# Performance work log

Hardware: AMD Instinct MI355X
Metric: run time of the kernel (lower is better)

The kernel has to match this reference:

```python
import jax, jax.numpy as jnp
import numpy as np

N, E, W_IN, W_OUT, NUM_CLASS, M = 4096, 5, 512, 128, 16, 1024
NUM_LAYERS, ALPHA, THETA = 64, 0.1, 0.5

def leaky_relu(x):
    return jnp.where(x >= 0, x, 0.01 * x)

def setup_inputs() -> dict:
    key = jax.random.key(0)
    ks = jax.random.split(key, 16)
    u = jax.random.uniform(ks[0], (N, N, E), jnp.float32)
    A = jnp.where(u < 0.01, u, 0.0)
    X = jax.random.normal(ks[1], (N, W_IN), jnp.float32)
    target_x = jax.random.randint(ks[2], (M,), 0, N)
    target = jax.random.randint(ks[3], (M,), 0, NUM_CLASS)
    def xav(k, shape):
        fan_in, fan_out = shape[-2], shape[-1]
        lim = (6.0 / (fan_in + fan_out)) ** 0.5
        return jax.random.uniform(k, shape, jnp.float32, -lim, lim)
    H0 = W_IN + E * W_OUT  # DGCN input width
    return dict(
        A=A, X=X, target_x=target_x, target=target,
        weight=xav(ks[4], (W_IN, W_OUT)),
        attw=xav(ks[5], (1, N)),
        attb=jnp.zeros((1, W_OUT), jnp.float32),
        attq=xav(ks[6], (1, W_OUT)),
        Wg=xav(ks[7], (W_IN, W_IN)), bg=jnp.zeros((W_IN,), jnp.float32),
        W0=xav(ks[8], (H0, W_OUT)), b0=jnp.zeros((W_OUT,), jnp.float32),
        Wconvs=xav(ks[9], (NUM_LAYERS, W_OUT, W_OUT)),
        Wd1=xav(ks[10], (W_OUT, W_OUT)), bd1=jnp.zeros((W_OUT,), jnp.float32),
        W1=xav(ks[11], (W_OUT, W_OUT)), b1=jnp.zeros((W_OUT,), jnp.float32),
        W2=xav(ks[12], (W_OUT, NUM_CLASS)), b2=jnp.zeros((NUM_CLASS,), jnp.float32),
    )

def reference(A, X, target_x, target, weight, attw, attb, attq, Wg, bg, W0, b0,
              Wconvs, Wd1, bd1, W1, b1, W2, b2):
    Ae = jnp.transpose(A, (2, 0, 1))              # [E,N,N]
    I = jnp.eye(N, dtype=A.dtype)
    # gcn_conv feature transform is identical for every edge type (dropout p=0)
    Xw = leaky_relu(leaky_relu(X @ Wg + bg) @ weight)   # [N, w_out]
    # norm(H, add=True): transpose, set diagonal to 1, row-normalize by degree
    Ht = Ae.transpose(0, 2, 1) * (1.0 - I) + I          # [E,N,N]
    deg = Ht.sum(-1)
    dinv = jnp.where(deg > 0, 1.0 / deg, 0.0)
    lgcn = jax.nn.relu(jnp.einsum('enm,md->end', dinv[..., None] * Ht, Xw))  # [E,N,w_out]
    # edge-type attention
    tm = jnp.tanh(jnp.einsum('n,end->ed', attw[0], lgcn) + attb)  # [E,w_out]
    watt = (tm * attq[0]).sum(-1)                                  # [E]
    beta = jax.nn.softmax(watt) * E
    Xcat = (beta[:, None, None] * lgcn).transpose(1, 0, 2).reshape(N, E * W_OUT)
    X_ = jnp.concatenate([Xcat, X], axis=1)       # [N, w_in + E*w_out]
    # DGCN: GCNII stack on binary nonzero pattern of mean adjacency, gcn_norm
    B = (jnp.mean(Ae, 0) != 0).astype(A.dtype)
    Bs = jnp.maximum(B, I)                        # add remaining self-loops
    d = Bs.sum(1)
    dis = jnp.where(d > 0, jax.lax.rsqrt(d), 0.0)
    A_hat = dis[:, None] * Bs * dis[None, :]      # D^-1/2 (B+I) D^-1/2
    x0 = jax.nn.relu(X_ @ W0 + b0)                # [N, w_out]
    betas_l = jnp.log(THETA / jnp.arange(1, NUM_LAYERS + 1, dtype=A.dtype) + 1.0)
    def step(x, inp):
        Wl, bl = inp
        h = A_hat @ x
        h = (1.0 - ALPHA) * h + ALPHA * x0        # initial residual
        x = jax.nn.relu((1.0 - bl) * h + bl * (h @ Wl))  # identity mapping
        return x, None
    x, _ = jax.lax.scan(step, x0, (Wconvs, betas_l))
    Z = leaky_relu(x @ Wd1 + bd1)                 # DGCN lins[1] + outer leaky_relu
    Z = leaky_relu(Z @ W1 + b1)                   # linear1
    y = Z[target_x] @ W2 + b2                     # linear2 on labeled nodes [M,C]
    logp = jax.nn.log_softmax(y, axis=-1)
    loss = -jnp.mean(jnp.take_along_axis(logp, target[:, None], axis=1))
    return loss, y
```

## Files before the change

kernel.cpp:

```cpp
#include <hip/hip_runtime.h>
#include <cstdint>
#include <cmath>

#define NN   4096
#define EE   5
#define WIN  512
#define WOUT 128
#define HH0  1152
#define NLAY 64
#define NCLS 16
#define MT   1024
#define GCAP 96
#define BCAP 320
#define ECAP 48
#define KSPLIT 8
#define KCHUNK 512
#define NTILE  8

typedef __attribute__((ext_vector_type(8))) short     bf16x8_t;
typedef __attribute__((ext_vector_type(8))) unsigned short ushort8_t;
typedef __attribute__((ext_vector_type(4))) float     f32x4_t;

__device__ inline unsigned short f2bf(float f) {
  unsigned int u = __float_as_uint(f);
  unsigned int r = (u + 0x7FFFu + ((u >> 16) & 1u)) >> 16;
  return (unsigned short)r;
}

__device__ __forceinline__ void gload16(const unsigned short* g, unsigned short* l) {
  __builtin_amdgcn_global_load_lds(
      (__attribute__((address_space(1))) void*)g,
      (__attribute__((address_space(3))) void*)l, 16, 0, 0);
}

__global__ __launch_bounds__(256) void gemm_kernel(
    const float* __restrict__ A, const float* __restrict__ W,
    const float* __restrict__ bias, float* __restrict__ C,
    int Mdim, int Kdim, int Ndim, int act) {
  __shared__ __align__(16) float sA[16][68];
  __shared__ __align__(16) float sW[16][64];
  int tid = threadIdx.x;
  int tx = tid & 15, ty = tid >> 4;
  int row0 = blockIdx.y * 64, col0 = blockIdx.x * 64;
  float acc[4][4] = {};
  int mA = tid >> 2;
  int kA = (tid & 3) << 2;
  int kW = tid >> 4;
  int nW = (tid & 15) << 2;
  for (int k0 = 0; k0 < Kdim; k0 += 16) {
    float4 av = *(const float4*)(A + (size_t)(row0 + mA) * Kdim + k0 + kA);
    float4 wv = *(const float4*)(W + (size_t)(k0 + kW) * Ndim + col0 + nW);
    sA[kA + 0][mA] = av.x;
    sA[kA + 1][mA] = av.y;
    sA[kA + 2][mA] = av.z;
    sA[kA + 3][mA] = av.w;
    *(float4*)&sW[kW][nW] = wv;
    __syncthreads();
#pragma unroll
    for (int kk = 0; kk < 16; kk++) {
      float4 a = *(const float4*)&sA[kk][ty << 2];
      float4 b = *(const float4*)&sW[kk][tx << 2];
      acc[0][0] += a.x * b.x; acc[0][1] += a.x * b.y; acc[0][2] += a.x * b.z; acc[0][3] += a.x * b.w;
      acc[1][0] += a.y * b.x; acc[1][1] += a.y * b.y; acc[1][2] += a.y * b.z; acc[1][3] += a.y * b.w;
      acc[2][0] += a.z * b.x; acc[2][1] += a.z * b.y; acc[2][2] += a.z * b.z; acc[2][3] += a.z * b.w;
      acc[3][0] += a.w * b.x; acc[3][1] += a.w * b.y; acc[3][2] += a.w * b.z; acc[3][3] += a.w * b.w;
    }
    __syncthreads();
  }
#pragma unroll
  for (int i = 0; i < 4; i++) {
    int r = row0 + (ty << 2) + i;
#pragma unroll
    for (int jc = 0; jc < 4; jc++) {
      int c = col0 + (tx << 2) + jc;
      float o = acc[i][jc];
      if (bias) o += bias[c];
      if (act == 1) o = fmaxf(o, 0.f);
      else if (act == 2) o = (o >= 0.f) ? o : 0.01f * o;
      C[(size_t)r * Ndim + c] = o;
    }
  }
}

__global__ __launch_bounds__(256) void scan_rows_kernel(
    const float* __restrict__ A, int* __restrict__ fcnt, int* __restrict__ fidx,
    float* __restrict__ fval, int* __restrict__ bcnt, int* __restrict__ bidx) {
  __shared__ int   lbuf[1024];
  __shared__ int   lcnt;
  __shared__ int   ecnt[EE];
  __shared__ int   en2[EE][ECAP];
  __shared__ float ev[EE][ECAP];
  __shared__ int   rbase;
  __shared__ int   gbase[EE];
  int tid = threadIdx.x;
  int n1 = blockIdx.x >> 2;
  int qb = (blockIdx.x & 3) << 10;
  if (tid == 0) lcnt = 0;
  if (tid < EE) ecnt[tid] = 0;
  __syncthreads();
  const float4* src = (const float4*)(A + ((size_t)n1 * NN + qb) * EE);
  float buf[20];
  float4* bf4 = (float4*)buf;
#pragma unroll
  for (int c = 0; c < 5; c++) bf4[c] = src[tid * 5 + c];
  int n2base = qb + tid * 4;
#pragma unroll
  for (int u = 0; u < 4; u++) {
    int n2 = n2base + u;
    if (n2 == n1) continue;
    bool any = false;
#pragma unroll
    for (int e = 0; e < EE; e++) {
      float v = buf[u * 5 + e];
      if (v != 0.f) {
        any = true;
        int s = atomicAdd(&ecnt[e], 1);
        if (s < ECAP) { en2[e][s] = n2; ev[e][s] = v; }
      }
    }
    if (any) {
      int s = atomicAdd(&lcnt, 1);
      lbuf[s] = n2;
    }
  }
  __syncthreads();
  if (tid == 0) rbase = atomicAdd(&bcnt[n1], lcnt);
  if (tid < EE) gbase[tid] = atomicAdd(&fcnt[tid * NN + n1], min(ecnt[tid], ECAP));
  __syncthreads();
  int c = lcnt, rb = rbase;
  for (int s = tid; s < c; s += 256)
    if (rb + s < BCAP) bidx[(size_t)n1 * BCAP + rb + s] = lbuf[s];
#pragma unroll
  for (int e = 0; e < EE; e++) {
    int ec = min(ecnt[e], ECAP), gb = gbase[e];
    size_t base = ((size_t)e * NN + n1) * GCAP;
    for (int s = tid; s < ec; s += 256) {
      if (gb + s < GCAP) {
        fidx[base + gb + s] = en2[e][s];
        fval[base + gb + s] = ev[e][s];
      }
    }
  }
}

__global__ __launch_bounds__(64) void transpose_kernel(
    const int* __restrict__ fcnt, const int* __restrict__ fidx, const float* __restrict__ fval,
    int* __restrict__ gcnt, int* __restrict__ gidx, float* __restrict__ gval) {
  int id = blockIdx.x;
  int n1 = id & (NN - 1);
  int e  = id >> 12;
  int c = min(fcnt[id], GCAP);
  for (int s = threadIdx.x; s < c; s += 64) {
    int   n2 = fidx[(size_t)id * GCAP + s];
    float v  = fval[(size_t)id * GCAP + s];
    int t = e * NN + n2;
    int slot = atomicAdd(&gcnt[t], 1);
    if (slot < GCAP) {
      gidx[(size_t)t * GCAP + slot] = n1;
      gval[(size_t)t * GCAP + slot] = v;
    }
  }
}

__global__ void dinv_dis_kernel(const int* __restrict__ gcnt, const float* __restrict__ gval,
                                float* __restrict__ dinv, const int* __restrict__ bcnt,
                                float* __restrict__ dis) {
  int t = blockIdx.x * 256 + threadIdx.x;
  if (t < EE * NN) {
    int cnt = min(gcnt[t], GCAP);
    float s = 1.0f;
    for (int k = 0; k < cnt; k++) s += gval[(size_t)t * GCAP + k];
    dinv[t] = 1.0f / s;
  }
  if (t < NN) dis[t] = rsqrtf(1.0f + (float)min(bcnt[t], BCAP));
}

__global__ __launch_bounds__(256) void build_ahat_kernel(
    const int* __restrict__ bcnt, const int* __restrict__ bidx,
    const float* __restrict__ dis, unsigned short* __restrict__ Ab) {
  __shared__ unsigned int bits[128];
  int i = blockIdx.x, t = threadIdx.x;
  if (t < 128) bits[t] = 0;
  __syncthreads();
  int cnt = min(bcnt[i], BCAP);
  for (int s = t; s < cnt; s += 256) {
    int j = bidx[(size_t)i * BCAP + s];
    atomicOr(&bits[j >> 5], 1u << (j & 31));
  }
  __syncthreads();
  float di = dis[i];
  int c0 = t * 16;
  unsigned short out[16];
#pragma unroll
  for (int u = 0; u < 16; u++) {
    int j = c0 + u;
    bool on = ((bits[j >> 5] >> (j & 31)) & 1u) || (j == i);
    out[u] = on ? f2bf(di * dis[j]) : (unsigned short)0;
  }
  *(ushort8_t*)&Ab[(size_t)i * NN + c0]     = *(ushort8_t*)&out[0];
  *(ushort8_t*)&Ab[(size_t)i * NN + c0 + 8] = *(ushort8_t*)&out[8];
}

__global__ __launch_bounds__(128) void lgcn_kernel(
    const int* __restrict__ gcnt, const int* __restrict__ gidx, const float* __restrict__ gval,
    const float* __restrict__ dinv, const float* __restrict__ Xw, float* __restrict__ lgcn) {
  int i = blockIdx.x, e = blockIdx.y, d = threadIdx.x;
  int t = e * NN + i;
  int cnt = min(gcnt[t], GCAP);
  __shared__ int   sj[GCAP];
  __shared__ float sv[GCAP];
  for (int s = d; s < cnt; s += 128) {
    sj[s] = gidx[(size_t)t * GCAP + s];
    sv[s] = gval[(size_t)t * GCAP + s];
  }
  __syncthreads();
  float acc = Xw[(size_t)i * WOUT + d];
  for (int s = 0; s < cnt; s++) acc += sv[s] * Xw[(size_t)sj[s] * WOUT + d];
  float r = dinv[t] * acc;
  lgcn[(size_t)t * WOUT + d] = fmaxf(r, 0.f);
}

__global__ void att_partial_kernel(const float* __restrict__ lgcn, const float* __restrict__ attw,
                                   float* __restrict__ tm_pre) {
  int e = blockIdx.y, d = threadIdx.x;
  int nbase = blockIdx.x * 128;
  float acc = 0.f;
  for (int k = 0; k < 128; k++) {
    int n = nbase + k;
    acc += attw[n] * lgcn[((size_t)(e * NN + n)) * WOUT + d];
  }
  atomicAdd(&tm_pre[e * WOUT + d], acc);
}

__global__ void att_final_kernel(const float* __restrict__ tm_pre, const float* __restrict__ attb,
                                 const float* __restrict__ attq, float* __restrict__ beta) {
  int lane = threadIdx.x;
  __shared__ float sw[EE];
  for (int e = 0; e < EE; e++) {
    float v = 0.f;
    for (int d = lane; d < WOUT; d += 64) {
      float tmv = tanhf(tm_pre[e * WOUT + d] + attb[d]);
      v += tmv * attq[d];
    }
    for (int off = 32; off; off >>= 1) v += __shfl_down(v, off, 64);
    if (lane == 0) sw[e] = v;
  }
  __syncthreads();
  if (lane == 0) {
    float mx = sw[0];
    for (int e = 1; e < EE; e++) mx = fmaxf(mx, sw[e]);
    float se = 0.f, ex[EE];
    for (int e = 0; e < EE; e++) { ex[e] = expf(sw[e] - mx); se += ex[e]; }
    for (int e = 0; e < EE; e++) beta[e] = ex[e] / se * (float)EE;
  }
}

__global__ void xcat_kernel(const float* __restrict__ lgcn, const float* __restrict__ X,
                            const float* __restrict__ beta, float* __restrict__ Xc) {
  int idx = blockIdx.x * 256 + threadIdx.x;
  const int total = NN * HH0;
  for (; idx < total; idx += gridDim.x * 256) {
    int n = idx / HH0, c = idx - n * HH0;
    float v;
    if (c < EE * WOUT) {
      int e = c >> 7, d = c & 127;
      v = beta[e] * lgcn[((size_t)(e * NN + n)) * WOUT + d];
    } else {
      v = X[(size_t)n * WIN + (c - EE * WOUT)];
    }
    Xc[idx] = v;
  }
}

__global__ __launch_bounds__(256) void xT_convert_kernel(
    const float* __restrict__ x, unsigned short* __restrict__ xT) {
  __shared__ float sh2[128][36];
  int r0 = blockIdx.x * 32, t = threadIdx.x;
  const float4* x4 = (const float4*)(x + (size_t)r0 * WOUT);
#pragma unroll
  for (int q = 0; q < 4; q++) {
    int lin = t + q * 256;
    int r = lin >> 5, c = (lin & 31) * 4;
    float4 v = x4[lin];
    sh2[c + 0][r] = v.x; sh2[c + 1][r] = v.y; sh2[c + 2][r] = v.z; sh2[c + 3][r] = v.w;
  }
  __syncthreads();
  int c = t >> 1, half = t & 1;
  unsigned short tmp[16];
#pragma unroll
  for (int rr = 0; rr < 16; rr++) tmp[rr] = f2bf(sh2[c][half * 16 + rr]);
  *(ushort8_t*)&xT[(size_t)c * NN + r0 + half * 16]     = *(ushort8_t*)&tmp[0];
  *(ushort8_t*)&xT[(size_t)c * NN + r0 + half * 16 + 8] = *(ushort8_t*)&tmp[8];
}

__global__ __launch_bounds__(256) void spmm_kernel(
    const unsigned short* __restrict__ Ab, const unsigned short* __restrict__ xbT,
    float* __restrict__ P) {
  __shared__ __align__(16) unsigned short sT[2][12288];
  int t = threadIdx.x;
  int rt = blockIdx.x & 63, kc = blockIdx.x >> 6;
  int r0 = rt * 64, k0 = kc * KCHUNK;
  int wave = t >> 6, lane = t & 63;
  int wr = (wave & 1) * 32, wc = (wave >> 1) * 64;
  int quad = lane >> 4, mrow = lane & 15;
  f32x4_t acc[2][4] = {};

  const unsigned short* gq[6];
  int lq[6];
#pragma unroll
  for (int q = 0; q < 6; q++) {
    int c = wave * 6 + q;
    if (c < 8) {
      int sub = c >> 2, rb = c & 3;
      gq[q] = Ab + (size_t)(r0 + rb * 16 + (lane >> 2)) * NN + k0 + sub * 32 + (lane & 3) * 8;
      lq[q] = sub * 2048 + rb * 512;
    } else {
      int cc = c - 8;
      int sub = cc >> 3, rb = cc & 7;
      gq[q] = xbT + (size_t)(rb * 16 + (lane >> 2)) * NN + k0 + sub * 32 + (lane & 3) * 8;
      lq[q] = 4096 + sub * 4096 + rb * 512;
    }
  }

#define STAGE(BUF, TS)                                         \
  {                                                            \
    unsigned short* lb = &sT[(BUF)][0];                        \
    _Pragma("unroll")                                          \
    for (int q = 0; q < 6; q++)                                \
      gload16(gq[q] + (TS) * 64, lb + lq[q]);                  \
  }

  STAGE(0, 0);
  asm volatile("s_waitcnt vmcnt(0)" ::: "memory");
  __builtin_amdgcn_s_barrier();

  int cur = 0;
  for (int tt = 0; tt < NTILE; tt++) {
    if (tt < NTILE - 1) STAGE(cur ^ 1, tt + 1);
    const unsigned short* base = &sT[cur][0];
    bf16x8_t af[2][2], bfv[2][4];
#pragma unroll
    for (int kk = 0; kk < 2; kk++) {
#pragma unroll
      for (int mi = 0; mi < 2; mi++)
        af[kk][mi] = *(const bf16x8_t*)&base[kk * 2048 + (wr + mi * 16 + mrow) * 32 + quad * 8];
#pragma unroll
      for (int nj = 0; nj < 4; nj++)
        bfv[kk][nj] = *(const bf16x8_t*)&base[4096 + kk * 4096 + (wc + nj * 16 + mrow) * 32 + quad * 8];
    }
#pragma unroll
    for (int kk = 0; kk < 2; kk++)
#pragma unroll
      for (int mi = 0; mi < 2; mi++)
#pragma unroll
        for (int nj = 0; nj < 4; nj++)
          acc[mi][nj] = __builtin_amdgcn_mfma_f32_16x16x32_bf16(af[kk][mi], bfv[kk][nj], acc[mi][nj], 0, 0, 0);
    if (tt < NTILE - 1) {
      asm volatile("s_waitcnt vmcnt(0)" ::: "memory");
      __builtin_amdgcn_s_barrier();
      cur ^= 1;
    }
  }
#undef STAGE

  float* Pk = P + (size_t)kc * (NN * WOUT);
#pragma unroll
  for (int mi = 0; mi < 2; mi++)
#pragma unroll
    for (int nj = 0; nj < 4; nj++) {
#pragma unroll
      for (int r4 = 0; r4 < 4; r4++) {
        int row = r0 + wr + mi * 16 + quad * 4 + r4;
        int col = wc + nj * 16 + mrow;
        Pk[(size_t)row * WOUT + col] = acc[mi][nj][r4];
      }
    }
}

__global__ __launch_bounds__(256) void gcnii_epi_kernel(
    const float* __restrict__ P, const float* __restrict__ x0,
    const float* __restrict__ Wl, float bl,
    float* __restrict__ xout_f32, unsigned short* __restrict__ xoutT, int write_f32) {
  __shared__ float sh2[128][22];
  int r0 = blockIdx.x * 16, t = threadIdx.x;
#pragma unroll
  for (int q = 0; q < 2; q++) {
    int lin = t + q * 256;
    int r = lin >> 5, c = (lin & 31) * 4;
    size_t base4 = ((size_t)(r0 + r) * WOUT + c) >> 2;
    float4 s = {0.f, 0.f, 0.f, 0.f};
#pragma unroll
    for (int kc = 0; kc < KSPLIT; kc++) {
      float4 p = ((const float4*)P)[(size_t)kc * (NN * WOUT / 4) + base4];
      s.x += p.x; s.y += p.y; s.z += p.z; s.w += p.w;
    }
    float4 xv = ((const float4*)x0)[base4];
    s.x = 0.9f * s.x + 0.1f * xv.x;
    s.y = 0.9f * s.y + 0.1f * xv.y;
    s.z = 0.9f * s.z + 0.1f * xv.z;
    s.w = 0.9f * s.w + 0.1f * xv.w;
    sh2[c + 0][r] = s.x; sh2[c + 1][r] = s.y; sh2[c + 2][r] = s.z; sh2[c + 3][r] = s.w;
  }
  __syncthreads();
  int tx = t & 31, ty = t >> 5;
  float2 hv[4];
#pragma unroll
  for (int j = 0; j < 4; j++) hv[j] = *(const float2*)&sh2[tx * 4 + j][ty * 2];
  float o[2][4] = {};
  for (int k = 0; k < WOUT; k++) {
    float2 a = *(const float2*)&sh2[k][ty * 2];
    float4 w = *(const float4*)&Wl[k * WOUT + tx * 4];
    o[0][0] += a.x * w.x; o[0][1] += a.x * w.y; o[0][2] += a.x * w.z; o[0][3] += a.x * w.w;
    o[1][0] += a.y * w.x; o[1][1] += a.y * w.y; o[1][2] += a.y * w.z; o[1][3] += a.y * w.w;
  }
  float c1 = 1.f - bl;
  float y[2][4];
  float hvv[2][4] = {{hv[0].x, hv[1].x, hv[2].x, hv[3].x},
                     {hv[0].y, hv[1].y, hv[2].y, hv[3].y}};
#pragma unroll
  for (int i = 0; i < 2; i++)
#pragma unroll
    for (int j = 0; j < 4; j++)
      y[i][j] = fmaxf(c1 * hvv[i][j] + bl * o[i][j], 0.f);
  if (write_f32) {
#pragma unroll
    for (int i = 0; i < 2; i++) {
      float4 v = {y[i][0], y[i][1], y[i][2], y[i][3]};
      *(float4*)&xout_f32[(size_t)(r0 + ty * 2 + i) * WOUT + tx * 4] = v;
    }
  }
  __syncthreads();
#pragma unroll
  for (int i = 0; i < 2; i++)
#pragma unroll
    for (int j = 0; j < 4; j++)
      sh2[tx * 4 + j][ty * 2 + i] = y[i][j];
  __syncthreads();
  int c = t >> 1, half = t & 1;
  unsigned short tmp[8];
#pragma unroll
  for (int rr = 0; rr < 8; rr++) tmp[rr] = f2bf(sh2[c][half * 8 + rr]);
  *(ushort8_t*)&xoutT[(size_t)c * NN + r0 + half * 8] = *(ushort8_t*)&tmp[0];
}

__global__ __launch_bounds__(256) void head_kernel(
    const float* __restrict__ Z, const int* __restrict__ txv, const int* __restrict__ tgt,
    const float* __restrict__ W2, const float* __restrict__ b2,
    float* __restrict__ out_y, float* __restrict__ lossp) {
  int tid = threadIdx.x;
  int mr = tid >> 4, c = tid & 15;
  int m = blockIdx.x * 16 + mr;
  const float* zr = Z + (size_t)txv[m] * WOUT;
  float acc = b2[c];
  for (int k = 0; k < WOUT; k++) acc += zr[k] * W2[k * NCLS + c];
  out_y[(size_t)m * NCLS + c] = acc;
  float mx = acc;
  for (int off = 8; off; off >>= 1) mx = fmaxf(mx, __shfl_xor(mx, off, 16));
  float ex = expf(acc - mx);
  float se = ex;
  for (int off = 8; off; off >>= 1) se += __shfl_xor(se, off, 16);
  float lse = mx + logf(se);
  float contrib = (c == tgt[m]) ? (lse - acc) : 0.f;
  __shared__ float red[256];
  red[tid] = contrib;
  __syncthreads();
  for (int stp = 128; stp; stp >>= 1) {
    if (tid < stp) red[tid] += red[tid + stp];
    __syncthreads();
  }
  if (tid == 0) lossp[blockIdx.x] = red[0];
}

__global__ void loss_final_kernel(const float* __restrict__ lossp, float* __restrict__ out_loss) {
  int lane = threadIdx.x;
  float v = (lane < 64) ? lossp[lane] : 0.f;
  for (int off = 32; off; off >>= 1) v += __shfl_down(v, off, 64);
  if (lane == 0) out_loss[0] = v / (float)MT;
}

extern "C" void kernel_launch(void* const* d_in, const int* in_sizes, int n_in,
                              void* d_out, int out_size, void* d_ws, size_t ws_size,
                              hipStream_t stream) {
  const float* A      = (const float*)d_in[0];
  const float* X      = (const float*)d_in[1];
  const int*   txv    = (const int*)d_in[2];
  const int*   tgt    = (const int*)d_in[3];
  const float* weight = (const float*)d_in[4];
  const float* attw   = (const float*)d_in[5];
  const float* attb   = (const float*)d_in[6];
  const float* attq   = (const float*)d_in[7];
  const float* Wg     = (const float*)d_in[8];
  const float* bg     = (const float*)d_in[9];
  const float* W0     = (const float*)d_in[10];
  const float* b0     = (const float*)d_in[11];
  const float* Wconvs = (const float*)d_in[12];
  const float* Wd1    = (const float*)d_in[13];
  const float* bd1    = (const float*)d_in[14];
  const float* W1     = (const float*)d_in[15];
  const float* b1     = (const float*)d_in[16];
  const float* W2     = (const float*)d_in[17];
  const float* b2     = (const float*)d_in[18];

  float* ws  = (float*)d_ws;
  int*   wsi = (int*)d_ws;

  const size_t O_GCNT  = 0;
  const size_t O_BCNT  = 20480;
  const size_t O_FCNT  = 24576;
  const size_t O_DINV  = 45056;
  const size_t O_DIS   = 65536;
  const size_t O_TMPRE = 69632;
  const size_t O_BETA  = 70272;
  const size_t O_LOSSP = 70288;
  const size_t O_GIDX  = 71680;
  const size_t O_GVAL  = O_GIDX + 1966080;
  const size_t O_FIDX  = O_GVAL + 1966080;
  const size_t O_FVAL  = O_FIDX + 1966080;
  const size_t O_BIDX  = O_FVAL + 1966080;
  const size_t O_LGCN  = O_BIDX + 1310720;
  const size_t O_XW    = O_LGCN + 2621440;
  const size_t O_X0    = O_XW   + 524288;
  const size_t O_XA    = O_X0   + 524288;
  const size_t O_XB    = O_XA   + 524288;
  const size_t O_AB    = O_XB   + 524288;
  const size_t O_XBT0  = O_AB   + 8388608;
  const size_t O_XBT1  = O_XBT0 + 262144;
  const size_t O_P     = O_XBT1 + 262144;
  const size_t O_T1    = O_FVAL;
  const size_t O_XCAT  = O_GIDX;

  hipMemsetAsync(ws + O_GCNT, 0, 45056 * 4, stream);
  hipMemsetAsync(ws + O_TMPRE, 0, 640 * 4, stream);

  dim3 blk(256);
  gemm_kernel<<<dim3(WIN / 64, NN / 64), blk, 0, stream>>>(X, Wg, bg, ws + O_T1, NN, WIN, WIN, 2);
  gemm_kernel<<<dim3(WOUT / 64, NN / 64), blk, 0, stream>>>(ws + O_T1, weight, nullptr, ws + O_XW, NN, WIN, WOUT, 2);
  scan_rows_kernel<<<NN * 4, 256, 0, stream>>>(A, wsi + O_FCNT, wsi + O_FIDX, ws + O_FVAL,
                                               wsi + O_BCNT, wsi + O_BIDX);
  transpose_kernel<<<EE * NN, 64, 0, stream>>>(wsi + O_FCNT, wsi + O_FIDX, ws + O_FVAL,
                                               wsi + O_GCNT, wsi + O_GIDX, ws + O_GVAL);
  dinv_dis_kernel<<<80, 256, 0, stream>>>(wsi + O_GCNT, ws + O_GVAL, ws + O_DINV,
                                          wsi + O_BCNT, ws + O_DIS);
  build_ahat_kernel<<<NN, 256, 0, stream>>>(wsi + O_BCNT, wsi + O_BIDX, ws + O_DIS,
                                            (unsigned short*)(ws + O_AB));
  lgcn_kernel<<<dim3(NN, EE), 128, 0, stream>>>(wsi + O_GCNT, wsi + O_GIDX, ws + O_GVAL,
                                                ws + O_DINV, ws + O_XW, ws + O_LGCN);
  att_partial_kernel<<<dim3(32, EE), 128, 0, stream>>>(ws + O_LGCN, attw, ws + O_TMPRE);
  att_final_kernel<<<1, 64, 0, stream>>>(ws + O_TMPRE, attb, attq, ws + O_BETA);
  xcat_kernel<<<4096, 256, 0, stream>>>(ws + O_LGCN, X, ws + O_BETA, ws + O_XCAT);
  gemm_kernel<<<dim3(WOUT / 64, NN / 64), blk, 0, stream>>>(ws + O_XCAT, W0, b0, ws + O_X0, NN, HH0, WOUT, 1);
  xT_convert_kernel<<<NN / 32, 256, 0, stream>>>(ws + O_X0, (unsigned short*)(ws + O_XBT0));
  for (int l = 0; l < NLAY; l++) {
    float bl = logf(0.5f / (float)(l + 1) + 1.0f);
    const unsigned short* xin = (const unsigned short*)(ws + ((l & 1) ? O_XBT1 : O_XBT0));
    unsigned short* xoT = (unsigned short*)(ws + ((l & 1) ? O_XBT0 : O_XBT1));
    spmm_kernel<<<64 * KSPLIT, 256, 0, stream>>>((const unsigned short*)(ws + O_AB), xin, ws + O_P);
    gcnii_epi_kernel<<<NN / 16, 256, 0, stream>>>(ws + O_P, ws + O_X0,
                                                  Wconvs + (size_t)l * WOUT * WOUT, bl,
                                                  ws + O_XA, xoT, (l == NLAY - 1) ? 1 : 0);
  }
  gemm_kernel<<<dim3(WOUT / 64, NN / 64), blk, 0, stream>>>(ws + O_XA, Wd1, bd1, ws + O_XB, NN, WOUT, WOUT, 2);
  gemm_kernel<<<dim3(WOUT / 64, NN / 64), blk, 0, stream>>>(ws + O_XB, W1, b1, ws + O_X0, NN, WOUT, WOUT, 2);
  head_kernel<<<MT / 16, 256, 0, stream>>>(ws + O_X0, txv, tgt, W2, b2,
                                           (float*)d_out + 1, ws + O_LOSSP);
  loss_final_kernel<<<1, 64, 0, stream>>>(ws + O_LOSSP, (float*)d_out);
}
```

Before: 2.386 ms.

## Replace dense bf16 A_hat with bitmap and fold D^-1/2 scaling into features

Instead of materializing the dense normalized adjacency in bf16 (32 MB) and streaming it every layer, the normalization D^-1/2 (B+I) D^-1/2 is factored. The binary pattern is stored as a 2 MB bitmap that the SpMM kernel expands into bf16 ones and zeros in shared memory, and the column scaling dis[j] is applied to x when writing the transposed bf16 input. The row scaling dis[i] is applied in the epilogue. This cuts the per-layer HBM traffic for A by about 16x, at the cost of extra ALU work for bitmap expansion and a full __syncthreads in place of the explicit waitcnt barrier.

```diff
diff --git a/kernel.cpp b/kernel.cpp
--- a/kernel.cpp
+++ b/kernel.cpp
@@ -175,9 +175,9 @@
   if (t < NN) dis[t] = rsqrtf(1.0f + (float)min(bcnt[t], BCAP));
 }
 
-__global__ __launch_bounds__(256) void build_ahat_kernel(
+__global__ __launch_bounds__(256) void build_bitmap_kernel(
     const int* __restrict__ bcnt, const int* __restrict__ bidx,
-    const float* __restrict__ dis, unsigned short* __restrict__ Ab) {
+    unsigned int* __restrict__ bm) {
   __shared__ unsigned int bits[128];
   int i = blockIdx.x, t = threadIdx.x;
   if (t < 128) bits[t] = 0;
@@ -187,18 +187,9 @@
     int j = bidx[(size_t)i * BCAP + s];
     atomicOr(&bits[j >> 5], 1u << (j & 31));
   }
-  __syncthreads();
-  float di = dis[i];
-  int c0 = t * 16;
-  unsigned short out[16];
-#pragma unroll
-  for (int u = 0; u < 16; u++) {
-    int j = c0 + u;
-    bool on = ((bits[j >> 5] >> (j & 31)) & 1u) || (j == i);
-    out[u] = on ? f2bf(di * dis[j]) : (unsigned short)0;
-  }
-  *(ushort8_t*)&Ab[(size_t)i * NN + c0]     = *(ushort8_t*)&out[0];
-  *(ushort8_t*)&Ab[(size_t)i * NN + c0 + 8] = *(ushort8_t*)&out[8];
+  if (t == 0) atomicOr(&bits[i >> 5], 1u << (i & 31));
+  __syncthreads();
+  if (t < 128) bm[(size_t)i * 128 + t] = bits[t];
 }
 
 __global__ __launch_bounds__(128) void lgcn_kernel(
@@ -273,9 +264,12 @@
 }
 
 __global__ __launch_bounds__(256) void xT_convert_kernel(
-    const float* __restrict__ x, unsigned short* __restrict__ xT) {
+    const float* __restrict__ x, const float* __restrict__ dis,
+    unsigned short* __restrict__ xT) {
   __shared__ float sh2[128][36];
+  __shared__ float sdis[32];
   int r0 = blockIdx.x * 32, t = threadIdx.x;
+  if (t < 32) sdis[t] = dis[r0 + t];
   const float4* x4 = (const float4*)(x + (size_t)r0 * WOUT);
 #pragma unroll
   for (int q = 0; q < 4; q++) {
@@ -288,65 +282,85 @@
   int c = t >> 1, half = t & 1;
   unsigned short tmp[16];
 #pragma unroll
-  for (int rr = 0; rr < 16; rr++) tmp[rr] = f2bf(sh2[c][half * 16 + rr]);
+  for (int rr = 0; rr < 16; rr++)
+    tmp[rr] = f2bf(sdis[half * 16 + rr] * sh2[c][half * 16 + rr]);
   *(ushort8_t*)&xT[(size_t)c * NN + r0 + half * 16]     = *(ushort8_t*)&tmp[0];
   *(ushort8_t*)&xT[(size_t)c * NN + r0 + half * 16 + 8] = *(ushort8_t*)&tmp[8];
 }
 
 __global__ __launch_bounds__(256) void spmm_kernel(
-    const unsigned short* __restrict__ Ab, const unsigned short* __restrict__ xbT,
+    const unsigned int* __restrict__ bm, const unsigned short* __restrict__ xbT,
     float* __restrict__ P) {
-  __shared__ __align__(16) unsigned short sT[2][12288];
+  __shared__ __align__(16) unsigned short sX[2][2][128 * 32];
+  __shared__ __align__(16) unsigned short sA[2][2][64 * 32];
+  __shared__ __align__(16) unsigned int   sBM[64][16];
   int t = threadIdx.x;
   int rt = blockIdx.x & 63, kc = blockIdx.x >> 6;
   int r0 = rt * 64, k0 = kc * KCHUNK;
   int wave = t >> 6, lane = t & 63;
   int wr = (wave & 1) * 32, wc = (wave >> 1) * 64;
   int quad = lane >> 4, mrow = lane & 15;
+  int er = t >> 2, eq = t & 3;
   f32x4_t acc[2][4] = {};
 
-  const unsigned short* gq[6];
-  int lq[6];
-#pragma unroll
-  for (int q = 0; q < 6; q++) {
-    int c = wave * 6 + q;
-    if (c < 8) {
-      int sub = c >> 2, rb = c & 3;
-      gq[q] = Ab + (size_t)(r0 + rb * 16 + (lane >> 2)) * NN + k0 + sub * 32 + (lane & 3) * 8;
-      lq[q] = sub * 2048 + rb * 512;
-    } else {
-      int cc = c - 8;
-      int sub = cc >> 3, rb = cc & 7;
-      gq[q] = xbT + (size_t)(rb * 16 + (lane >> 2)) * NN + k0 + sub * 32 + (lane & 3) * 8;
-      lq[q] = 4096 + sub * 4096 + rb * 512;
-    }
-  }
-
-#define STAGE(BUF, TS)                                         \
-  {                                                            \
-    unsigned short* lb = &sT[(BUF)][0];                        \
-    _Pragma("unroll")                                          \
-    for (int q = 0; q < 6; q++)                                \
-      gload16(gq[q] + (TS) * 64, lb + lq[q]);                  \
-  }
-
-  STAGE(0, 0);
-  asm volatile("s_waitcnt vmcnt(0)" ::: "memory");
-  __builtin_amdgcn_s_barrier();
+  {
+    uint4 v = *(const uint4*)&bm[(size_t)(r0 + er) * 128 + (k0 >> 5) + eq * 4];
+    *(uint4*)&sBM[er][eq * 4] = v;
+  }
+
+  const unsigned short* gXq[4];
+  int loff[4];
+#pragma unroll
+  for (int q = 0; q < 4; q++) {
+    int cc = wave * 4 + q;
+    int sub = cc >> 3, rb = cc & 7;
+    gXq[q] = xbT + (size_t)(rb * 16 + (lane >> 2)) * NN + k0 + sub * 32 + (lane & 3) * 8;
+    loff[q] = sub * 4096 + rb * 512;
+  }
+  unsigned short* sXf = &sX[0][0][0];
+
+#define STAGE_X(BUF, TS)                                                  \
+  {                                                                       \
+    _Pragma("unroll")                                                     \
+    for (int q = 0; q < 4; q++)                                           \
+      gload16(gXq[q] + (TS) * 64, sXf + (BUF) * 8192 + loff[q]);          \
+  }
+
+#define EXPA(BUF, TT)                                                     \
+  {                                                                       \
+    unsigned dw = sBM[er][(TT) * 2 + (eq >> 1)];                          \
+    unsigned bits = (dw >> ((eq & 1) * 16)) & 0xFFFFu;                    \
+    unsigned o[8];                                                        \
+    _Pragma("unroll")                                                     \
+    for (int u = 0; u < 8; u++) {                                         \
+      unsigned w = (bits & (1u << (2 * u))) ? 0x3F80u : 0u;               \
+      if (bits & (1u << (2 * u + 1))) w |= 0x3F800000u;                   \
+      o[u] = w;                                                           \
+    }                                                                     \
+    unsigned short* dst = &sA[(BUF)][eq >> 1][er * 32 + (eq & 1) * 16];   \
+    *(uint4*)dst = make_uint4(o[0], o[1], o[2], o[3]);                    \
+    *(uint4*)(dst + 8) = make_uint4(o[4], o[5], o[6], o[7]);              \
+  }
+
+  STAGE_X(0, 0);
+  EXPA(0, 0);
+  __syncthreads();
 
   int cur = 0;
   for (int tt = 0; tt < NTILE; tt++) {
-    if (tt < NTILE - 1) STAGE(cur ^ 1, tt + 1);
-    const unsigned short* base = &sT[cur][0];
+    if (tt < NTILE - 1) {
+      STAGE_X(cur ^ 1, tt + 1);
+      EXPA(cur ^ 1, tt + 1);
+    }
     bf16x8_t af[2][2], bfv[2][4];
 #pragma unroll
     for (int kk = 0; kk < 2; kk++) {
 #pragma unroll
       for (int mi = 0; mi < 2; mi++)
-        af[kk][mi] = *(const bf16x8_t*)&base[kk * 2048 + (wr + mi * 16 + mrow) * 32 + quad * 8];
+        af[kk][mi] = *(const bf16x8_t*)&sA[cur][kk][(wr + mi * 16 + mrow) * 32 + quad * 8];
 #pragma unroll
       for (int nj = 0; nj < 4; nj++)
-        bfv[kk][nj] = *(const bf16x8_t*)&base[4096 + kk * 4096 + (wc + nj * 16 + mrow) * 32 + quad * 8];
+        bfv[kk][nj] = *(const bf16x8_t*)&sX[cur][kk][(wc + nj * 16 + mrow) * 32 + quad * 8];
     }
 #pragma unroll
     for (int kk = 0; kk < 2; kk++)
@@ -356,12 +370,12 @@
         for (int nj = 0; nj < 4; nj++)
           acc[mi][nj] = __builtin_amdgcn_mfma_f32_16x16x32_bf16(af[kk][mi], bfv[kk][nj], acc[mi][nj], 0, 0, 0);
     if (tt < NTILE - 1) {
-      asm volatile("s_waitcnt vmcnt(0)" ::: "memory");
-      __builtin_amdgcn_s_barrier();
+      __syncthreads();
       cur ^= 1;
     }
   }
-#undef STAGE
+#undef STAGE_X
+#undef EXPA
 
   float* Pk = P + (size_t)kc * (NN * WOUT);
 #pragma unroll
@@ -379,14 +393,17 @@
 
 __global__ __launch_bounds__(256) void gcnii_epi_kernel(
     const float* __restrict__ P, const float* __restrict__ x0,
-    const float* __restrict__ Wl, float bl,
+    const float* __restrict__ Wl, float bl, const float* __restrict__ dis,
     float* __restrict__ xout_f32, unsigned short* __restrict__ xoutT, int write_f32) {
   __shared__ float sh2[128][22];
+  __shared__ float sdis[16];
   int r0 = blockIdx.x * 16, t = threadIdx.x;
+  if (t < 16) sdis[t] = dis[r0 + t];
 #pragma unroll
   for (int q = 0; q < 2; q++) {
     int lin = t + q * 256;
     int r = lin >> 5, c = (lin & 31) * 4;
+    float dr = dis[r0 + r];
     size_t base4 = ((size_t)(r0 + r) * WOUT + c) >> 2;
     float4 s = {0.f, 0.f, 0.f, 0.f};
 #pragma unroll
@@ -395,10 +412,11 @@
       s.x += p.x; s.y += p.y; s.z += p.z; s.w += p.w;
     }
     float4 xv = ((const float4*)x0)[base4];
-    s.x = 0.9f * s.x + 0.1f * xv.x;
-    s.y = 0.9f * s.y + 0.1f * xv.y;
-    s.z = 0.9f * s.z + 0.1f * xv.z;
-    s.w = 0.9f * s.w + 0.1f * xv.w;
+    float sc = 0.9f * dr;
+    s.x = sc * s.x + 0.1f * xv.x;
+    s.y = sc * s.y + 0.1f * xv.y;
+    s.z = sc * s.z + 0.1f * xv.z;
+    s.w = sc * s.w + 0.1f * xv.w;
     sh2[c + 0][r] = s.x; sh2[c + 1][r] = s.y; sh2[c + 2][r] = s.z; sh2[c + 3][r] = s.w;
   }
   __syncthreads();
@@ -439,7 +457,8 @@
   int c = t >> 1, half = t & 1;
   unsigned short tmp[8];
 #pragma unroll
-  for (int rr = 0; rr < 8; rr++) tmp[rr] = f2bf(sh2[c][half * 8 + rr]);
+  for (int rr = 0; rr < 8; rr++)
+    tmp[rr] = f2bf(sdis[half * 8 + rr] * sh2[c][half * 8 + rr]);
   *(ushort8_t*)&xoutT[(size_t)c * NN + r0 + half * 8] = *(ushort8_t*)&tmp[0];
 }
 
@@ -522,8 +541,8 @@
   const size_t O_X0    = O_XW   + 524288;
   const size_t O_XA    = O_X0   + 524288;
   const size_t O_XB    = O_XA   + 524288;
-  const size_t O_AB    = O_XB   + 524288;
-  const size_t O_XBT0  = O_AB   + 8388608;
+  const size_t O_BM    = O_XB   + 524288;
+  const size_t O_XBT0  = O_BM   + 524288;
   const size_t O_XBT1  = O_XBT0 + 262144;
   const size_t O_P     = O_XBT1 + 262144;
   const size_t O_T1    = O_FVAL;
@@ -541,23 +560,25 @@
                                                wsi + O_GCNT, wsi + O_GIDX, ws + O_GVAL);
   dinv_dis_kernel<<<80, 256, 0, stream>>>(wsi + O_GCNT, ws + O_GVAL, ws + O_DINV,
                                           wsi + O_BCNT, ws + O_DIS);
-  build_ahat_kernel<<<NN, 256, 0, stream>>>(wsi + O_BCNT, wsi + O_BIDX, ws + O_DIS,
-                                            (unsigned short*)(ws + O_AB));
+  build_bitmap_kernel<<<NN, 256, 0, stream>>>(wsi + O_BCNT, wsi + O_BIDX,
+                                              (unsigned int*)(ws + O_BM));
   lgcn_kernel<<<dim3(NN, EE), 128, 0, stream>>>(wsi + O_GCNT, wsi + O_GIDX, ws + O_GVAL,
                                                 ws + O_DINV, ws + O_XW, ws + O_LGCN);
   att_partial_kernel<<<dim3(32, EE), 128, 0, stream>>>(ws + O_LGCN, attw, ws + O_TMPRE);
   att_final_kernel<<<1, 64, 0, stream>>>(ws + O_TMPRE, attb, attq, ws + O_BETA);
   xcat_kernel<<<4096, 256, 0, stream>>>(ws + O_LGCN, X, ws + O_BETA, ws + O_XCAT);
   gemm_kernel<<<dim3(WOUT / 64, NN / 64), blk, 0, stream>>>(ws + O_XCAT, W0, b0, ws + O_X0, NN, HH0, WOUT, 1);
-  xT_convert_kernel<<<NN / 32, 256, 0, stream>>>(ws + O_X0, (unsigned short*)(ws + O_XBT0));
+  xT_convert_kernel<<<NN / 32, 256, 0, stream>>>(ws + O_X0, ws + O_DIS,
+                                                 (unsigned short*)(ws + O_XBT0));
   for (int l = 0; l < NLAY; l++) {
     float bl = logf(0.5f / (float)(l + 1) + 1.0f);
     const unsigned short* xin = (const unsigned short*)(ws + ((l & 1) ? O_XBT1 : O_XBT0));
     unsigned short* xoT = (unsigned short*)(ws + ((l & 1) ? O_XBT0 : O_XBT1));
-    spmm_kernel<<<64 * KSPLIT, 256, 0, stream>>>((const unsigned short*)(ws + O_AB), xin, ws + O_P);
+    spmm_kernel<<<64 * KSPLIT, 256, 0, stream>>>((const unsigned int*)(ws + O_BM), xin, ws + O_P);
     gcnii_epi_kernel<<<NN / 16, 256, 0, stream>>>(ws + O_P, ws + O_X0,
                                                   Wconvs + (size_t)l * WOUT * WOUT, bl,
-                                                  ws + O_XA, xoT, (l == NLAY - 1) ? 1 : 0);
+                                                  ws + O_DIS, ws + O_XA, xoT,
+                                                  (l == NLAY - 1) ? 1 : 0);
   }
   gemm_kernel<<<dim3(WOUT / 64, NN / 64), blk, 0, stream>>>(ws + O_XA, Wd1, bd1, ws + O_XB, NN, WOUT, WOUT, 2);
   gemm_kernel<<<dim3(WOUT / 64, NN / 64), blk, 0, stream>>>(ws + O_XB, W1, b1, ws + O_X0, NN, WOUT, WOUT, 2);
```

Result: slower. 2.656 ms (+11.3%).

## Fuse GCNII epilogue into split-K SpMM via last-block atomic counter

Applied to the files above, without the earlier changes.

Merges the per-layer SpMM and GCNII epilogue kernels into one launch. Each of the KSPLIT blocks for a row tile writes its partial result and increments a per-layer, per-tile atomic counter. The last block to arrive reduces the partials and runs the residual, Wl matmul, ReLU and bf16 transpose for 64 rows in four 16-row groups. This removes 64 kernel launches and their gaps, but the epilogue now runs on only 64 blocks instead of 256, which reduces its parallelism.

```diff
diff --git a/kernel.cpp b/kernel.cpp
--- a/kernel.cpp
+++ b/kernel.cpp
@@ -293,10 +293,15 @@
   *(ushort8_t*)&xT[(size_t)c * NN + r0 + half * 16 + 8] = *(ushort8_t*)&tmp[8];
 }
 
-__global__ __launch_bounds__(256) void spmm_kernel(
+#define SUBSZ (128 * 32)
+__global__ __launch_bounds__(256) void spmm_epi_kernel(
     const unsigned short* __restrict__ Ab, const unsigned short* __restrict__ xbT,
-    float* __restrict__ P) {
+    float* __restrict__ P, int* __restrict__ cnt,
+    const float* __restrict__ x0, const float* __restrict__ Wl, float bl,
+    float* __restrict__ xout_f32, unsigned short* __restrict__ xoutT, int write_f32) {
   __shared__ __align__(16) unsigned short sT[2][12288];
+  __shared__ float sh2[128][22];
+  __shared__ int slast;
   int t = threadIdx.x;
   int rt = blockIdx.x & 63, kc = blockIdx.x >> 6;
   int r0 = rt * 64, k0 = kc * KCHUNK;
@@ -375,72 +380,77 @@
         Pk[(size_t)row * WOUT + col] = acc[mi][nj][r4];
       }
     }
-}
-
-__global__ __launch_bounds__(256) void gcnii_epi_kernel(
-    const float* __restrict__ P, const float* __restrict__ x0,
-    const float* __restrict__ Wl, float bl,
-    float* __restrict__ xout_f32, unsigned short* __restrict__ xoutT, int write_f32) {
-  __shared__ float sh2[128][22];
-  int r0 = blockIdx.x * 16, t = threadIdx.x;
-#pragma unroll
-  for (int q = 0; q < 2; q++) {
-    int lin = t + q * 256;
-    int r = lin >> 5, c = (lin & 31) * 4;
-    size_t base4 = ((size_t)(r0 + r) * WOUT + c) >> 2;
-    float4 s = {0.f, 0.f, 0.f, 0.f};
-#pragma unroll
-    for (int kc = 0; kc < KSPLIT; kc++) {
-      float4 p = ((const float4*)P)[(size_t)kc * (NN * WOUT / 4) + base4];
-      s.x += p.x; s.y += p.y; s.z += p.z; s.w += p.w;
-    }
-    float4 xv = ((const float4*)x0)[base4];
-    s.x = 0.9f * s.x + 0.1f * xv.x;
-    s.y = 0.9f * s.y + 0.1f * xv.y;
-    s.z = 0.9f * s.z + 0.1f * xv.z;
-    s.w = 0.9f * s.w + 0.1f * xv.w;
-    sh2[c + 0][r] = s.x; sh2[c + 1][r] = s.y; sh2[c + 2][r] = s.z; sh2[c + 3][r] = s.w;
-  }
-  __syncthreads();
-  int tx = t & 31, ty = t >> 5;
-  float2 hv[4];
-#pragma unroll
-  for (int j = 0; j < 4; j++) hv[j] = *(const float2*)&sh2[tx * 4 + j][ty * 2];
-  float o[2][4] = {};
-  for (int k = 0; k < WOUT; k++) {
-    float2 a = *(const float2*)&sh2[k][ty * 2];
-    float4 w = *(const float4*)&Wl[k * WOUT + tx * 4];
-    o[0][0] += a.x * w.x; o[0][1] += a.x * w.y; o[0][2] += a.x * w.z; o[0][3] += a.x * w.w;
-    o[1][0] += a.y * w.x; o[1][1] += a.y * w.y; o[1][2] += a.y * w.z; o[1][3] += a.y * w.w;
-  }
+
+  __threadfence();
+  __syncthreads();
+  if (t == 0) slast = (atomicAdd(&cnt[rt], 1) == KSPLIT - 1) ? 1 : 0;
+  __syncthreads();
+  if (!slast) return;
+  __threadfence();
+
   float c1 = 1.f - bl;
-  float y[2][4];
-  float hvv[2][4] = {{hv[0].x, hv[1].x, hv[2].x, hv[3].x},
-                     {hv[0].y, hv[1].y, hv[2].y, hv[3].y}};
-#pragma unroll
-  for (int i = 0; i < 2; i++)
-#pragma unroll
-    for (int j = 0; j < 4; j++)
-      y[i][j] = fmaxf(c1 * hvv[i][j] + bl * o[i][j], 0.f);
-  if (write_f32) {
-#pragma unroll
-    for (int i = 0; i < 2; i++) {
-      float4 v = {y[i][0], y[i][1], y[i][2], y[i][3]};
-      *(float4*)&xout_f32[(size_t)(r0 + ty * 2 + i) * WOUT + tx * 4] = v;
-    }
-  }
-  __syncthreads();
-#pragma unroll
-  for (int i = 0; i < 2; i++)
-#pragma unroll
-    for (int j = 0; j < 4; j++)
-      sh2[tx * 4 + j][ty * 2 + i] = y[i][j];
-  __syncthreads();
-  int c = t >> 1, half = t & 1;
-  unsigned short tmp[8];
-#pragma unroll
-  for (int rr = 0; rr < 8; rr++) tmp[rr] = f2bf(sh2[c][half * 8 + rr]);
-  *(ushort8_t*)&xoutT[(size_t)c * NN + r0 + half * 8] = *(ushort8_t*)&tmp[0];
+#pragma unroll 1
+  for (int g = 0; g < 4; g++) {
+    int e0 = r0 + g * 16;
+#pragma unroll
+    for (int q = 0; q < 2; q++) {
+      int lin = t + q * 256;
+      int r = lin >> 5, cl = (lin & 31) * 4;
+      size_t base4 = ((size_t)(e0 + r) * WOUT + cl) >> 2;
+      float4 s = {0.f, 0.f, 0.f, 0.f};
+#pragma unroll
+      for (int k2 = 0; k2 < KSPLIT; k2++) {
+        float4 p = ((const float4*)P)[(size_t)k2 * (NN * WOUT / 4) + base4];
+        s.x += p.x; s.y += p.y; s.z += p.z; s.w += p.w;
+      }
+      float4 xv = ((const float4*)x0)[base4];
+      s.x = 0.9f * s.x + 0.1f * xv.x;
+      s.y = 0.9f * s.y + 0.1f * xv.y;
+      s.z = 0.9f * s.z + 0.1f * xv.z;
+      s.w = 0.9f * s.w + 0.1f * xv.w;
+      sh2[cl + 0][r] = s.x; sh2[cl + 1][r] = s.y; sh2[cl + 2][r] = s.z; sh2[cl + 3][r] = s.w;
+    }
+    __syncthreads();
+    int tx2 = t & 31, ty2 = t >> 5;
+    float2 hv[4];
+#pragma unroll
+    for (int j = 0; j < 4; j++) hv[j] = *(const float2*)&sh2[tx2 * 4 + j][ty2 * 2];
+    float o[2][4] = {};
+    for (int k = 0; k < WOUT; k++) {
+      float2 a = *(const float2*)&sh2[k][ty2 * 2];
+      float4 w = *(const float4*)&Wl[k * WOUT + tx2 * 4];
+      o[0][0] += a.x * w.x; o[0][1] += a.x * w.y; o[0][2] += a.x * w.z; o[0][3] += a.x * w.w;
+      o[1][0] += a.y * w.x; o[1][1] += a.y * w.y; o[1][2] += a.y * w.z; o[1][3] += a.y * w.w;
+    }
+    float y[2][4];
+    float hvv[2][4] = {{hv[0].x, hv[1].x, hv[2].x, hv[3].x},
+                       {hv[0].y, hv[1].y, hv[2].y, hv[3].y}};
+#pragma unroll
+    for (int i = 0; i < 2; i++)
+#pragma unroll
+      for (int j = 0; j < 4; j++)
+        y[i][j] = fmaxf(c1 * hvv[i][j] + bl * o[i][j], 0.f);
+    if (write_f32) {
+#pragma unroll
+      for (int i = 0; i < 2; i++) {
+        float4 v = {y[i][0], y[i][1], y[i][2], y[i][3]};
+        *(float4*)&xout_f32[(size_t)(e0 + ty2 * 2 + i) * WOUT + tx2 * 4] = v;
+      }
+    }
+    __syncthreads();
+#pragma unroll
+    for (int i = 0; i < 2; i++)
+#pragma unroll
+      for (int j = 0; j < 4; j++)
+        sh2[tx2 * 4 + j][ty2 * 2 + i] = y[i][j];
+    __syncthreads();
+    int cc = t >> 1, half = t & 1;
+    unsigned short tmp[8];
+#pragma unroll
+    for (int rr = 0; rr < 8; rr++) tmp[rr] = f2bf(sh2[cc][half * 8 + rr]);
+    *(ushort8_t*)&xoutT[(size_t)cc * NN + e0 + half * 8] = *(ushort8_t*)&tmp[0];
+    __syncthreads();
+  }
 }
 
 __global__ __launch_bounds__(256) void head_kernel(
@@ -526,11 +536,13 @@
   const size_t O_XBT0  = O_AB   + 8388608;
   const size_t O_XBT1  = O_XBT0 + 262144;
   const size_t O_P     = O_XBT1 + 262144;
+  const size_t O_CNT   = O_P    + 4194304;
   const size_t O_T1    = O_FVAL;
   const size_t O_XCAT  = O_GIDX;
 
   hipMemsetAsync(ws + O_GCNT, 0, 45056 * 4, stream);
   hipMemsetAsync(ws + O_TMPRE, 0, 640 * 4, stream);
+  hipMemsetAsync(ws + O_CNT, 0, 4096 * 4, stream);
 
   dim3 blk(256);
   gemm_kernel<<<dim3(WIN / 64, NN / 64), blk, 0, stream>>>(X, Wg, bg, ws + O_T1, NN, WIN, WIN, 2);
@@ -554,10 +566,10 @@
     float bl = logf(0.5f / (float)(l + 1) + 1.0f);
     const unsigned short* xin = (const unsigned short*)(ws + ((l & 1) ? O_XBT1 : O_XBT0));
     unsigned short* xoT = (unsigned short*)(ws + ((l & 1) ? O_XBT0 : O_XBT1));
-    spmm_kernel<<<64 * KSPLIT, 256, 0, stream>>>((const unsigned short*)(ws + O_AB), xin, ws + O_P);
-    gcnii_epi_kernel<<<NN / 16, 256, 0, stream>>>(ws + O_P, ws + O_X0,
-                                                  Wconvs + (size_t)l * WOUT * WOUT, bl,
-                                                  ws + O_XA, xoT, (l == NLAY - 1) ? 1 : 0);
+    spmm_epi_kernel<<<64 * KSPLIT, 256, 0, stream>>>(
+        (const unsigned short*)(ws + O_AB), xin, ws + O_P, wsi + O_CNT + l * 64,
+        ws + O_X0, Wconvs + (size_t)l * WOUT * WOUT, bl,
+        ws + O_XA, xoT, (l == NLAY - 1) ? 1 : 0);
   }
   gemm_kernel<<<dim3(WOUT / 64, NN / 64), blk, 0, stream>>>(ws + O_XA, Wd1, bd1, ws + O_XB, NN, WOUT, WOUT, 2);
   gemm_kernel<<<dim3(WOUT / 64, NN / 64), blk, 0, stream>>>(ws + O_XB, W1, b1, ws + O_X0, NN, WOUT, WOUT, 2);
```

After: 7.051 ms. 195% more time.
